# Kernel optimization log

Hardware: AMD Instinct MI355X
Metric: run time of the kernel (lower is better)

Reference implementation:

```python
import jax, jax.numpy as jnp
import numpy as np

# class_mask_range after __init__ normalization: first range (-1,1) => min=-1, max=1,
# so the rescale 2*(x-min)/(max-min)-1 is the identity on all ranges.
RANGES = [(-1.0, 1.0), (-1.0, -0.5), (-0.5, 0.0), (0.0, 0.5), (0.5, 1.0)]
N_CLASSES = len(RANGES)
WEIGHTS = [1.0 / N_CLASSES] * N_CLASSES  # class_weight [1]*5 normalized by its sum


def setup_inputs() -> dict:
    key = jax.random.key(0)
    k1, k2 = jax.random.split(key)
    shape = (16, 1, 1024, 1024)
    return {
        "pre_img": jax.random.normal(k1, shape, dtype=jnp.float32),
        "real_img": jax.random.normal(k2, shape, dtype=jnp.float32),
    }


def reference(pre_img, real_img):
    # |pre*mask - real*mask| == mask * |pre - real| for 0/1 masks
    diff = jnp.abs(pre_img - real_img)
    class_mask = jnp.zeros(real_img.shape, dtype=jnp.int32)
    single_class_losses = []
    for i, (lb, ub) in enumerate(RANGES):
        m = (real_img >= lb) & (real_img <= ub)
        # later ranges overwrite earlier assignments, as in the torch loop
        class_mask = jnp.where(m, jnp.int32(i), class_mask)
        counts = m.sum()
        masked_sum = jnp.where(m, diff, 0.0).sum()
        denom = jnp.maximum(counts, 1).astype(diff.dtype)
        loss_i = jnp.where(counts == 0, 0.0, masked_sum / denom) * WEIGHTS[i]
        single_class_losses.append(loss_i)
    loss = sum(single_class_losses)
    class_mask_out = 2.0 * class_mask.astype(jnp.float32) / (N_CLASSES - 1) - 1.0
    return loss, jnp.stack(single_class_losses), class_mask_out
```

## Files before the change

kernel.cpp:

```cpp
#include <hip/hip_runtime.h>


#define N_BANKS 64
#define BANK_F  16

__device__ __forceinline__ void proc_elem(float pv, float rv,
                                          float s[5], unsigned int c[5],
                                          float& ov) {
    float d = fabsf(pv - rv);
    bool geM1  = rv >= -1.0f;
    bool leM05 = rv <= -0.5f;
    bool geM05 = rv >= -0.5f;
    bool le0   = rv <=  0.0f;
    bool ge0   = rv >=  0.0f;
    bool le05  = rv <=  0.5f;
    bool ge05  = rv >=  0.5f;
    bool le1   = rv <=  1.0f;
    bool in0 = geM1  && le1;
    bool in1 = geM1  && leM05;
    bool in2 = geM05 && le0;
    bool in3 = ge0   && le05;
    bool in4 = ge05  && le1;
    s[0] += in0 ? d : 0.f;  c[0] += in0;
    s[1] += in1 ? d : 0.f;  c[1] += in1;
    s[2] += in2 ? d : 0.f;  c[2] += in2;
    s[3] += in3 ? d : 0.f;  c[3] += in3;
    s[4] += in4 ? d : 0.f;  c[4] += in4;
    int cls = in4 ? 4 : (in3 ? 3 : (in2 ? 2 : (in1 ? 1 : 0)));
    ov = 0.5f * (float)cls - 1.0f;
}

__device__ __forceinline__ void proc_group(int i, const float4& p, const float4& r,
                                           float s[5], unsigned int c[5],
                                           float* __restrict__ mask_out) {
    float ov[4];
    proc_elem(p.x, r.x, s, c, ov[0]);
    proc_elem(p.y, r.y, s, c, ov[1]);
    proc_elem(p.z, r.z, s, c, ov[2]);
    proc_elem(p.w, r.w, s, c, ov[3]);
    float2* mo = (float2*)(mask_out + 4 * (size_t)i);
    mo[0] = make_float2(ov[0], ov[1]);
    mo[1] = make_float2(ov[2], ov[3]);
}

__global__ __launch_bounds__(256, 8) void mcl_main(
    const float* __restrict__ pre, const float* __restrict__ real,
    float* __restrict__ mask_out, float* __restrict__ acc, int n4, int n)
{
    float s[5] = {0.f, 0.f, 0.f, 0.f, 0.f};
    unsigned int c[5] = {0u, 0u, 0u, 0u, 0u};

    const int t = threadIdx.x;
    const int i0 = blockIdx.x * 512 + t;
    const int i1 = i0 + 256;
    const bool v0 = i0 < n4;
    const bool v1 = i1 < n4;

    const float4* pre4  = (const float4*)pre;
    const float4* real4 = (const float4*)real;

    float4 p0, r0, p1, r1;
    if (v0) { p0 = pre4[i0]; r0 = real4[i0]; }
    if (v1) { p1 = pre4[i1]; r1 = real4[i1]; }

    if (v0) proc_group(i0, p0, r0, s, c, mask_out);
    if (v1) proc_group(i1, p1, r1, s, c, mask_out);

    {
        int tail_base = n4 * 4;
        int tail = n - tail_base;
        int gtid = blockIdx.x * blockDim.x + t;
        if (gtid < tail) {
            int idx = tail_base + gtid;
            float ov;
            proc_elem(pre[idx], real[idx], s, c, ov);
            mask_out[idx] = ov;
        }
    }

#pragma unroll
    for (int j = 0; j < 5; ++j) {
#pragma unroll
        for (int off = 32; off > 0; off >>= 1) {
            s[j] += __shfl_down(s[j], off, 64);
            c[j] += __shfl_down(c[j], off, 64);
        }
    }

    __shared__ float ls[4][5];
    __shared__ unsigned int lc[4][5];
    int lane = t & 63;
    int wave = t >> 6;
    if (lane == 0) {
#pragma unroll
        for (int j = 0; j < 5; ++j) { ls[wave][j] = s[j]; lc[wave][j] = c[j]; }
    }
    __syncthreads();
    if (t < 5) {
        float ssum = ls[0][t] + ls[1][t] + ls[2][t] + ls[3][t];
        unsigned int csum = lc[0][t] + lc[1][t] + lc[2][t] + lc[3][t];
        float* bank = acc + (blockIdx.x & (N_BANKS - 1)) * BANK_F;
        atomicAdd(&bank[t], ssum);
        atomicAdd((unsigned int*)bank + 8 + t, csum);
    }
}

__global__ void mcl_final(const float* __restrict__ acc, float* __restrict__ out)
{
    int l = threadIdx.x;
    const float* bank = acc + l * BANK_F;
    float s[5];
    unsigned int c[5];
#pragma unroll
    for (int j = 0; j < 5; ++j) {
        s[j] = bank[j];
        c[j] = ((const unsigned int*)bank)[8 + j];
    }
#pragma unroll
    for (int j = 0; j < 5; ++j) {
#pragma unroll
        for (int off = 32; off > 0; off >>= 1) {
            s[j] += __shfl_down(s[j], off, 64);
            c[j] += __shfl_down(c[j], off, 64);
        }
    }
    if (l == 0) {
        float total = 0.f;
#pragma unroll
        for (int j = 0; j < 5; ++j) {
            unsigned int cnt = c[j];
            unsigned int denom = cnt > 1u ? cnt : 1u;
            float lv = (cnt == 0u) ? 0.f : (s[j] / (float)denom) * 0.2f;
            out[1 + j] = lv;
            total += lv;
        }
        out[0] = total;
    }
}

extern "C" void kernel_launch(void* const* d_in, const int* in_sizes, int n_in,
                              void* d_out, int out_size, void* d_ws, size_t ws_size,
                              hipStream_t stream) {
    const float* pre  = (const float*)d_in[0];
    const float* real = (const float*)d_in[1];
    float* out = (float*)d_out;
    int n = in_sizes[0];
    int n4 = n / 4;

    float* acc = (float*)d_ws;

    (void)hipMemsetAsync(d_ws, 0, N_BANKS * BANK_F * sizeof(float), stream);

    int blocks = (n4 + 511) / 512;
    if (blocks < 1) blocks = 1;
    mcl_main<<<blocks, 256, 0, stream>>>(pre, real, out + 6, acc, n4, n);
    mcl_final<<<1, 64, 0, stream>>>(acc, out);
}
```

Measured before the change: 176.3 us.

## Process eight float4 groups per thread with nontemporal mask stores and float counters

```diff
diff --git a/kernel.cpp b/kernel.cpp
--- a/kernel.cpp
+++ b/kernel.cpp
@@ -1,12 +1,17 @@
 #include <hip/hip_runtime.h>
 
 
-#define N_BANKS 64
+#define N_BANKS 256
 #define BANK_F  16
+#define TPB     256
+#define GROUPS  8
+#define SPAN    (TPB * GROUPS)
+
+typedef float nfloat2 __attribute__((ext_vector_type(2)));
 
 __device__ __forceinline__ void proc_elem(float pv, float rv,
-                                          float s[5], unsigned int c[5],
-                                          float& ov) {
+                                          float s[5], float c[5], float& ov)
+{
     float d = fabsf(pv - rv);
     bool geM1  = rv >= -1.0f;
     bool leM05 = rv <= -0.5f;
@@ -21,55 +26,60 @@
     bool in2 = geM05 && le0;
     bool in3 = ge0   && le05;
     bool in4 = ge05  && le1;
-    s[0] += in0 ? d : 0.f;  c[0] += in0;
-    s[1] += in1 ? d : 0.f;  c[1] += in1;
-    s[2] += in2 ? d : 0.f;  c[2] += in2;
-    s[3] += in3 ? d : 0.f;  c[3] += in3;
-    s[4] += in4 ? d : 0.f;  c[4] += in4;
-    int cls = in4 ? 4 : (in3 ? 3 : (in2 ? 2 : (in1 ? 1 : 0)));
-    ov = 0.5f * (float)cls - 1.0f;
+    s[0] += in0 ? d : 0.f;  c[0] += in0 ? 1.f : 0.f;
+    s[1] += in1 ? d : 0.f;  c[1] += in1 ? 1.f : 0.f;
+    s[2] += in2 ? d : 0.f;  c[2] += in2 ? 1.f : 0.f;
+    s[3] += in3 ? d : 0.f;  c[3] += in3 ? 1.f : 0.f;
+    s[4] += in4 ? d : 0.f;  c[4] += in4 ? 1.f : 0.f;
+    ov = in4 ? 1.0f : (in3 ? 0.5f : (in2 ? 0.0f : (in1 ? -0.5f : -1.0f)));
 }
 
 __device__ __forceinline__ void proc_group(int i, const float4& p, const float4& r,
-                                           float s[5], unsigned int c[5],
-                                           float* __restrict__ mask_out) {
-    float ov[4];
-    proc_elem(p.x, r.x, s, c, ov[0]);
-    proc_elem(p.y, r.y, s, c, ov[1]);
-    proc_elem(p.z, r.z, s, c, ov[2]);
-    proc_elem(p.w, r.w, s, c, ov[3]);
-    float2* mo = (float2*)(mask_out + 4 * (size_t)i);
-    mo[0] = make_float2(ov[0], ov[1]);
-    mo[1] = make_float2(ov[2], ov[3]);
+                                           float s[5], float c[5],
+                                           float* __restrict__ mask_out)
+{
+    float ov0, ov1, ov2, ov3;
+    proc_elem(p.x, r.x, s, c, ov0);
+    proc_elem(p.y, r.y, s, c, ov1);
+    proc_elem(p.z, r.z, s, c, ov2);
+    proc_elem(p.w, r.w, s, c, ov3);
+    nfloat2* mo = (nfloat2*)(mask_out + 4 * (size_t)i);
+    nfloat2 a; a.x = ov0; a.y = ov1;
+    nfloat2 b; b.x = ov2; b.y = ov3;
+    __builtin_nontemporal_store(a, mo);
+    __builtin_nontemporal_store(b, mo + 1);
 }
 
-__global__ __launch_bounds__(256, 8) void mcl_main(
+__global__ __launch_bounds__(TPB, 8) void mcl_main(
     const float* __restrict__ pre, const float* __restrict__ real,
     float* __restrict__ mask_out, float* __restrict__ acc, int n4, int n)
 {
     float s[5] = {0.f, 0.f, 0.f, 0.f, 0.f};
-    unsigned int c[5] = {0u, 0u, 0u, 0u, 0u};
+    float c[5] = {0.f, 0.f, 0.f, 0.f, 0.f};
 
     const int t = threadIdx.x;
-    const int i0 = blockIdx.x * 512 + t;
-    const int i1 = i0 + 256;
-    const bool v0 = i0 < n4;
-    const bool v1 = i1 < n4;
+    const int base = blockIdx.x * SPAN + t;
 
     const float4* pre4  = (const float4*)pre;
     const float4* real4 = (const float4*)real;
 
-    float4 p0, r0, p1, r1;
-    if (v0) { p0 = pre4[i0]; r0 = real4[i0]; }
-    if (v1) { p1 = pre4[i1]; r1 = real4[i1]; }
-
-    if (v0) proc_group(i0, p0, r0, s, c, mask_out);
-    if (v1) proc_group(i1, p1, r1, s, c, mask_out);
+#pragma unroll
+    for (int k = 0; k < GROUPS; k += 2) {
+        int i0 = base + k * TPB;
+        int i1 = i0 + TPB;
+        bool v0 = i0 < n4;
+        bool v1 = i1 < n4;
+        float4 p0, r0, p1, r1;
+        if (v0) { p0 = pre4[i0]; r0 = real4[i0]; }
+        if (v1) { p1 = pre4[i1]; r1 = real4[i1]; }
+        if (v0) proc_group(i0, p0, r0, s, c, mask_out);
+        if (v1) proc_group(i1, p1, r1, s, c, mask_out);
+    }
 
     {
         int tail_base = n4 * 4;
         int tail = n - tail_base;
-        int gtid = blockIdx.x * blockDim.x + t;
+        int gtid = blockIdx.x * TPB + t;
         if (gtid < tail) {
             int idx = tail_base + gtid;
             float ov;
@@ -88,7 +98,7 @@
     }
 
     __shared__ float ls[4][5];
-    __shared__ unsigned int lc[4][5];
+    __shared__ float lc[4][5];
     int lane = t & 63;
     int wave = t >> 6;
     if (lane == 0) {
@@ -96,41 +106,41 @@
         for (int j = 0; j < 5; ++j) { ls[wave][j] = s[j]; lc[wave][j] = c[j]; }
     }
     __syncthreads();
-    if (t < 5) {
-        float ssum = ls[0][t] + ls[1][t] + ls[2][t] + ls[3][t];
-        unsigned int csum = lc[0][t] + lc[1][t] + lc[2][t] + lc[3][t];
-        float* bank = acc + (blockIdx.x & (N_BANKS - 1)) * BANK_F;
-        atomicAdd(&bank[t], ssum);
-        atomicAdd((unsigned int*)bank + 8 + t, csum);
+    if (t < 10) {
+        int j = (t < 5) ? t : t - 5;
+        float v = (t < 5) ? (ls[0][j] + ls[1][j] + ls[2][j] + ls[3][j])
+                          : (lc[0][j] + lc[1][j] + lc[2][j] + lc[3][j]);
+        float* bank = acc + (size_t)(blockIdx.x & (N_BANKS - 1)) * BANK_F;
+        atomicAdd(&bank[t], v);
     }
 }
 
 __global__ void mcl_final(const float* __restrict__ acc, float* __restrict__ out)
 {
     int l = threadIdx.x;
-    const float* bank = acc + l * BANK_F;
-    float s[5];
-    unsigned int c[5];
+    float sum[10];
 #pragma unroll
-    for (int j = 0; j < 5; ++j) {
-        s[j] = bank[j];
-        c[j] = ((const unsigned int*)bank)[8 + j];
+    for (int j = 0; j < 10; ++j) sum[j] = 0.f;
+#pragma unroll
+    for (int b = 0; b < N_BANKS / 64; ++b) {
+        const float* bank = acc + (size_t)(b * 64 + l) * BANK_F;
+#pragma unroll
+        for (int j = 0; j < 10; ++j) sum[j] += bank[j];
     }
 #pragma unroll
-    for (int j = 0; j < 5; ++j) {
+    for (int j = 0; j < 10; ++j) {
 #pragma unroll
         for (int off = 32; off > 0; off >>= 1) {
-            s[j] += __shfl_down(s[j], off, 64);
-            c[j] += __shfl_down(c[j], off, 64);
+            sum[j] += __shfl_down(sum[j], off, 64);
         }
     }
     if (l == 0) {
         float total = 0.f;
 #pragma unroll
         for (int j = 0; j < 5; ++j) {
-            unsigned int cnt = c[j];
-            unsigned int denom = cnt > 1u ? cnt : 1u;
-            float lv = (cnt == 0u) ? 0.f : (s[j] / (float)denom) * 0.2f;
+            float cnt = sum[5 + j];
+            float denom = cnt > 1.f ? cnt : 1.f;
+            float lv = (cnt == 0.f) ? 0.f : (sum[j] / denom) * 0.2f;
             out[1 + j] = lv;
             total += lv;
         }
@@ -151,8 +161,8 @@
 
     (void)hipMemsetAsync(d_ws, 0, N_BANKS * BANK_F * sizeof(float), stream);
 
-    int blocks = (n4 + 511) / 512;
+    int blocks = (n4 + SPAN - 1) / SPAN;
     if (blocks < 1) blocks = 1;
-    mcl_main<<<blocks, 256, 0, stream>>>(pre, real, out + 6, acc, n4, n);
+    mcl_main<<<blocks, TPB, 0, stream>>>(pre, real, out + 6, acc, n4, n);
     mcl_final<<<1, 64, 0, stream>>>(acc, out);
 }
```

Measured after the change: 183.1 us. +3.9%, slower.
